# Kernel optimization log

Hardware: AMD Instinct MI355X
Metric: run time of the kernel (lower is better)

The kernel has to match this reference:

```python
import jax, jax.numpy as jnp
import numpy as np

DIM = 1024
HEADS = 16
DIM_HEAD = 64
INNER = HEADS * DIM_HEAD
THETA = 10000.0
EPS = 1e-5


def setup_inputs() -> dict:
    key = jax.random.key(0)
    k1, k2, k3, k4 = jax.random.split(key, 4)
    b, n = 4, 2048
    x = jax.random.normal(k1, (b, n, DIM), dtype=jnp.float32)
    gamma = jnp.ones((DIM,), jnp.float32)
    beta = jnp.zeros((DIM,), jnp.float32)
    w_qkv = jax.random.normal(k2, (DIM, 3 * INNER), dtype=jnp.float32) * (DIM ** -0.5)
    w_out = jax.random.normal(k3, (INNER, DIM), dtype=jnp.float32) * (INNER ** -0.5)
    b_out = jax.random.normal(k4, (DIM,), dtype=jnp.float32) * 0.01
    return {"x": x, "gamma": gamma, "beta": beta, "w_qkv": w_qkv, "w_out": w_out, "b_out": b_out}


def _rope_cos_sin(n, d, dtype):
    # freqs_cis = exp(i * t * theta^{-2j/d}) for j in [0, d/2)
    inv = 1.0 / (THETA ** (jnp.arange(0, d, 2, dtype=jnp.float32) / d))  # (d/2,)
    ang = jnp.arange(n, dtype=jnp.float32)[:, None] * inv[None, :]       # (n, d/2)
    return jnp.cos(ang).astype(dtype), jnp.sin(ang).astype(dtype)


def _apply_rope(t, cos, sin):
    # t: (b, n, h, d); rotate adjacent pairs along d
    b, n, h, d = t.shape
    tr = t.reshape(b, n, h, d // 2, 2)
    e, o = tr[..., 0], tr[..., 1]
    c = cos[None, :, None, :]
    s = sin[None, :, None, :]
    out = jnp.stack([e * c - o * s, e * s + o * c], axis=-1)
    return out.reshape(b, n, h, d)


def reference(x, gamma, beta, w_qkv, w_out, b_out):
    b, n, _ = x.shape
    # LayerNorm
    mu = jnp.mean(x, axis=-1, keepdims=True)
    var = jnp.mean(jnp.square(x - mu), axis=-1, keepdims=True)
    xn = (x - mu) * jax.lax.rsqrt(var + EPS) * gamma + beta
    # QKV projection (no bias)
    qkv = xn @ w_qkv  # (b, n, 3*INNER)
    q, k, v = jnp.split(qkv, 3, axis=-1)
    q = q.reshape(b, n, HEADS, DIM_HEAD)
    k = k.reshape(b, n, HEADS, DIM_HEAD)
    v = v.reshape(b, n, HEADS, DIM_HEAD)
    # RoPE on q, k (per head, global_start_pos = 0)
    cos, sin = _rope_cos_sin(n, DIM_HEAD, x.dtype)
    q = _apply_rope(q, cos, sin)
    k = _apply_rope(k, cos, sin)
    # attention
    scale = DIM_HEAD ** -0.5
    dots = jnp.einsum('bnhd,bmhd->bhnm', q, k) * scale
    attn = jax.nn.softmax(dots, axis=-1)
    out = jnp.einsum('bhnm,bmhd->bnhd', attn, v).reshape(b, n, INNER)
    return out @ w_out + b_out
```

## Files before the change

kernel.cpp:

```cpp
#include <hip/hip_runtime.h>
#include <hip/hip_fp16.h>

typedef __attribute__((ext_vector_type(8))) short short8;
typedef __attribute__((ext_vector_type(4))) short short4v;
typedef __attribute__((ext_vector_type(4))) float floatx4;
typedef _Float16 half8 __attribute__((ext_vector_type(8)));
typedef __fp16 fp16x2 __attribute__((ext_vector_type(2)));
typedef __attribute__((ext_vector_type(4))) unsigned uintx4;

extern "C" __device__ float __ocml_native_exp2_f32(float);

static __device__ __forceinline__ short f2h(float f) {
    _Float16 h = (_Float16)f;
    return __builtin_bit_cast(short, h);
}

static __device__ __forceinline__ unsigned pkrtz(float a, float b) {
    fp16x2 h = __builtin_amdgcn_cvt_pkrtz(a, b);
    return __builtin_bit_cast(unsigned, h);
}

static __device__ __forceinline__ void drain_all() { __builtin_amdgcn_s_waitcnt(0); }

static __device__ __forceinline__ floatx4 mfma16(short8 a, short8 b, floatx4 c) {
    return __builtin_amdgcn_mfma_f32_16x16x32_f16(__builtin_bit_cast(half8, a),
                                                  __builtin_bit_cast(half8, b), c, 0, 0, 0);
}

static __device__ __forceinline__ void async16(const void* g, void* l) {
    __builtin_amdgcn_global_load_lds((const __attribute__((address_space(1))) void*)g,
                                     (__attribute__((address_space(3))) void*)l, 16, 0, 0);
}

__global__ __launch_bounds__(256) void ln_kernel(const float* __restrict__ x,
                                                 const float* __restrict__ gamma,
                                                 const float* __restrict__ beta,
                                                 short* __restrict__ xh) {
    __shared__ float red[8];
    const int row = blockIdx.x, tid = threadIdx.x;
    const int w = tid >> 6, lane = tid & 63;
    const float4 v = ((const float4*)(x + (size_t)row * 1024))[tid];
    float s = v.x + v.y + v.z + v.w;
    float ss = v.x * v.x + v.y * v.y + v.z * v.z + v.w * v.w;
#pragma unroll
    for (int off = 32; off; off >>= 1) {
        s += __shfl_xor(s, off);
        ss += __shfl_xor(ss, off);
    }
    if (lane == 0) { red[w] = s; red[4 + w] = ss; }
    __syncthreads();
    s = red[0] + red[1] + red[2] + red[3];
    ss = red[4] + red[5] + red[6] + red[7];
    const float mu = s * (1.f / 1024.f);
    const float rs = rsqrtf(ss * (1.f / 1024.f) - mu * mu + 1e-5f);
    const float4 g = ((const float4*)gamma)[tid];
    const float4 bt = ((const float4*)beta)[tid];
    short4v ph;
    ph[0] = f2h((v.x - mu) * rs * g.x + bt.x);
    ph[1] = f2h((v.y - mu) * rs * g.y + bt.y);
    ph[2] = f2h((v.z - mu) * rs * g.z + bt.z);
    ph[3] = f2h((v.w - mu) * rs * g.w + bt.w);
    *(short4v*)(xh + (size_t)row * 1024 + tid * 4) = ph;
}

__global__ void tcast_h(const float* __restrict__ in, short* __restrict__ out, int R, int C) {
    __shared__ float t[32][33];
    const int bx = blockIdx.x * 32, by = blockIdx.y * 32;
    const int tx = threadIdx.x, ty = threadIdx.y;
#pragma unroll
    for (int i = 0; i < 32; i += 8) t[ty + i][tx] = in[(size_t)(by + ty + i) * C + bx + tx];
    __syncthreads();
#pragma unroll
    for (int i = 0; i < 32; i += 8) out[(size_t)(bx + ty + i) * R + by + tx] = f2h(t[tx][ty + i]);
}

__global__ __launch_bounds__(256, 4) void gemm_qkv(const short* __restrict__ A,
                                                   const short* __restrict__ BT,
                                                   short* __restrict__ Qd, short* __restrict__ Kd,
                                                   short* __restrict__ VTb) {
    extern __shared__ __align__(16) short pool[];
    short* sOut = pool;

    const int tid = threadIdx.x;
    const int w = tid >> 6, lane = tid & 63, quad = lane >> 4, l15 = lane & 15;
    const int wm = w >> 1, wn = w & 1;
    const int m0 = blockIdx.y * 128, n0 = blockIdx.x * 128;
    const int qsw = (quad ^ ((l15 >> 1) & 3)) * 8;

    int sr[2], skc[2];
#pragma unroll
    for (int i = 0; i < 2; ++i) {
        int c = i * 256 + tid;
        sr[i] = c >> 2;
        skc[i] = ((c & 3) ^ ((sr[i] >> 1) & 3)) << 3;
    }

    floatx4 acc[4][4];
#pragma unroll
    for (int i = 0; i < 4; i++)
#pragma unroll
        for (int j = 0; j < 4; j++) acc[i][j] = (floatx4){0.f, 0.f, 0.f, 0.f};

#pragma unroll
    for (int i = 0; i < 2; ++i) {
        int c = i * 256 + tid;
        async16(A + (size_t)(m0 + sr[i]) * 1024 + skc[i], (char*)pool + c * 16);
        async16(BT + (size_t)(n0 + sr[i]) * 1024 + skc[i], (char*)(pool + 4096) + c * 16);
    }
    drain_all();
    __syncthreads();

    for (int kt = 0; kt < 32; ++kt) {
        const short* cA = pool + (kt & 1) * 8192;
        const short* cB = cA + 4096;
        if (kt + 1 < 32) {
            short* nA = pool + ((kt + 1) & 1) * 8192;
            const int k0 = (kt + 1) * 32;
#pragma unroll
            for (int i = 0; i < 2; ++i) {
                int c = i * 256 + tid;
                async16(A + (size_t)(m0 + sr[i]) * 1024 + k0 + skc[i], (char*)nA + c * 16);
                async16(BT + (size_t)(n0 + sr[i]) * 1024 + k0 + skc[i], (char*)(nA + 4096) + c * 16);
            }
        }
        short8 af[4], bf[4];
#pragma unroll
        for (int t = 0; t < 4; t++) {
            af[t] = *(const short8*)(cA + (wm * 64 + t * 16 + l15) * 32 + qsw);
            bf[t] = *(const short8*)(cB + (wn * 64 + t * 16 + l15) * 32 + qsw);
        }
#pragma unroll
        for (int tm = 0; tm < 4; tm++)
#pragma unroll
            for (int tn = 0; tn < 4; tn++) acc[tm][tn] = mfma16(af[tm], bf[tn], acc[tm][tn]);
        drain_all();
        __syncthreads();
    }

    const int b = m0 >> 11, nnb = m0 & 2047;
    const bool isV = (n0 >= 2048);
    if (!isV) {
        const float qs = (n0 < 1024) ? 0.18033688011112042f : 1.0f;
#pragma unroll
        for (int tn = 0; tn < 4; tn++) {
            const int d = tn * 16 + l15;
            const int colL = wn * 64 + tn * 16 + l15;
            const float inv = exp2f((float)(d >> 1) * -0.4152410118609203f);
#pragma unroll
            for (int tm = 0; tm < 4; tm++) {
                const int rowL = wm * 64 + tm * 16 + quad * 4;
#pragma unroll
                for (int i = 0; i < 4; i++) {
                    float v = acc[tm][tn][i];
                    float pv = __shfl_xor(v, 1);
                    float ang = (float)(nnb + rowL + i) * inv;
                    float sn = __sinf(ang), cs = __cosf(ang);
                    float r = (d & 1) ? (pv * sn + v * cs) : (v * cs - pv * sn);
                    sOut[(rowL + i) * 136 + colL] = f2h(r * qs);
                }
            }
        }
        __syncthreads();
        short* dst0 = (n0 < 1024) ? Qd : Kd;
        const int hbase = (n0 & 1023) >> 6;
#pragma unroll
        for (int it = 0; it < 8; ++it) {
            int c = it * 256 + tid;
            int r = c >> 4, cg = (c & 15) * 8;
            int h = hbase + (cg >> 6), d = cg & 63;
            *(short8*)(dst0 + ((size_t)((b * 16 + h) * 2048 + nnb + r)) * 64 + d) =
                *(const short8*)(sOut + r * 136 + cg);
        }
    } else {
#pragma unroll
        for (int tn = 0; tn < 4; tn++) {
            const int colL = wn * 64 + tn * 16 + l15;
#pragma unroll
            for (int tm = 0; tm < 4; tm++) {
                const int rowL = wm * 64 + tm * 16 + quad * 4;
#pragma unroll
                for (int i = 0; i < 4; i++)
                    sOut[colL * 136 + rowL + i] = f2h(acc[tm][tn][i]);
            }
        }
        __syncthreads();
        const int hbase = (n0 & 1023) >> 6;
#pragma unroll
        for (int it = 0; it < 8; ++it) {
            int c = it * 256 + tid;
            int ci = c >> 4, rg = (c & 15) * 8;
            int h = hbase + (ci >> 6), d = ci & 63;
            short8 v = *(const short8*)(sOut + ci * 136 + rg);
            if (d & 8) v = __builtin_shufflevector(v, v, 4, 5, 6, 7, 0, 1, 2, 3);
            *(short8*)(VTb + ((size_t)((b * 16 + h) * 64 + d)) * 2048 + nnb + rg) = v;
        }
    }
}

__global__ __launch_bounds__(256, 4) void gemm_out(const short* __restrict__ A,
                                                   const short* __restrict__ BT,
                                                   float* __restrict__ Fout,
                                                   const float* __restrict__ bias) {
    __shared__ __align__(16) short pool2[16384];
    const int tid = threadIdx.x;
    const int w = tid >> 6, lane = tid & 63, quad = lane >> 4, l15 = lane & 15;
    const int wm = w >> 1, wn = w & 1;
    const int m0 = blockIdx.y * 128, n0 = blockIdx.x * 128;
    const int qsw = (quad ^ ((l15 >> 1) & 3)) * 8;

    int sr[2], skc[2];
#pragma unroll
    for (int i = 0; i < 2; ++i) {
        int c = i * 256 + tid;
        sr[i] = c >> 2;
        skc[i] = ((c & 3) ^ ((sr[i] >> 1) & 3)) << 3;
    }

    floatx4 acc[4][4];
#pragma unroll
    for (int i = 0; i < 4; i++)
#pragma unroll
        for (int j = 0; j < 4; j++) acc[i][j] = (floatx4){0.f, 0.f, 0.f, 0.f};

#pragma unroll
    for (int i = 0; i < 2; ++i) {
        int c = i * 256 + tid;
        async16(A + (size_t)(m0 + sr[i]) * 1024 + skc[i], (char*)pool2 + c * 16);
        async16(BT + (size_t)(n0 + sr[i]) * 1024 + skc[i], (char*)(pool2 + 4096) + c * 16);
    }
    drain_all();
    __syncthreads();

    for (int kt = 0; kt < 32; ++kt) {
        const short* cA = pool2 + (kt & 1) * 8192;
        const short* cB = cA + 4096;
        if (kt + 1 < 32) {
            short* nA = pool2 + ((kt + 1) & 1) * 8192;
            const int k0 = (kt + 1) * 32;
#pragma unroll
            for (int i = 0; i < 2; ++i) {
                int c = i * 256 + tid;
                async16(A + (size_t)(m0 + sr[i]) * 1024 + k0 + skc[i], (char*)nA + c * 16);
                async16(BT + (size_t)(n0 + sr[i]) * 1024 + k0 + skc[i], (char*)(nA + 4096) + c * 16);
            }
        }
        short8 af[4], bf[4];
#pragma unroll
        for (int t = 0; t < 4; t++) af[t] = *(const short8*)(cA + (wm * 64 + t * 16 + l15) * 32 + qsw);
#pragma unroll
        for (int t = 0; t < 4; t++) bf[t] = *(const short8*)(cB + (wn * 64 + t * 16 + l15) * 32 + qsw);
#pragma unroll
        for (int tm = 0; tm < 4; tm++)
#pragma unroll
            for (int tn = 0; tn < 4; tn++) acc[tm][tn] = mfma16(af[tm], bf[tn], acc[tm][tn]);
        drain_all();
        __syncthreads();
    }

#pragma unroll
    for (int tn = 0; tn < 4; tn++) {
        const int col = n0 + wn * 64 + tn * 16 + l15;
        const float bb = bias[col];
#pragma unroll
        for (int tm = 0; tm < 4; tm++) {
            const int row0 = m0 + wm * 64 + tm * 16 + quad * 4;
#pragma unroll
            for (int i = 0; i < 4; i++) Fout[(size_t)(row0 + i) * 1024 + col] = acc[tm][tn][i] + bb;
        }
    }
}

__global__ __launch_bounds__(512, 4) void attn_kernel(const short* __restrict__ Qg,
                                                      const short* __restrict__ Kg,
                                                      const short* __restrict__ VTg,
                                                      short* __restrict__ Og) {
    extern __shared__ __align__(16) short apool[];
    short* sKV0 = apool;
    short* sKV1 = apool + 8192;

    const int tid = threadIdx.x;
    const int w = tid >> 6, lane = tid & 63, quad = lane >> 4, l15 = lane & 15;
    const int qt = blockIdx.x, bh = blockIdx.y;

    const short* Qp = Qg + (size_t)(bh * 2048 + qt * 256) * 64;
    const short* Kp = Kg + (size_t)bh * 2048 * 64;
    const short* Vp = VTg + (size_t)bh * 64 * 2048;

    const int str = tid >> 3, stc = tid & 7;
    const int scl = stc ^ (str & 7);
    const int kSrcOff = str * 64 + scl * 8;
    const int vSrcOff = str * 2048 + scl * 8;
    const int dstOff = tid * 16;

    short8 aq[2][2];
#pragma unroll
    for (int rb = 0; rb < 2; rb++)
#pragma unroll
        for (int kh = 0; kh < 2; kh++)
            aq[rb][kh] = *(const short8*)(Qp + (w * 32 + rb * 16 + l15) * 64 + kh * 32 + quad * 8);

    short8 ones;
#pragma unroll
    for (int j = 0; j < 8; j++) ones[j] = 0x3C00;

    floatx4 o4[2][4], ol[2];
#pragma unroll
    for (int rb = 0; rb < 2; rb++) {
#pragma unroll
        for (int dt = 0; dt < 4; dt++) o4[rb][dt] = (floatx4){0.f, 0.f, 0.f, 0.f};
        ol[rb] = (floatx4){0.f, 0.f, 0.f, 0.f};
    }

    async16(Kp + kSrcOff, (char*)sKV0 + dstOff);
    async16(Vp + vSrcOff, (char*)(sKV0 + 4096) + dstOff);

    const int swz0 = (quad ^ (l15 & 7)) << 3;
    const int swz1 = ((4 | quad) ^ (l15 & 7)) << 3;

    for (int kt = 0; kt < 32; ++kt) {
        const short* sK = (kt & 1) ? sKV1 : sKV0;
        const short* sVT = sK + 4096;
        drain_all();
        __syncthreads();
        if (kt + 1 < 32) {
            short* nK = (kt & 1) ? sKV0 : sKV1;
            const int n0 = (kt + 1) * 64;
            async16(Kp + (size_t)n0 * 64 + kSrcOff, (char*)nK + dstOff);
            async16(Vp + n0 + vSrcOff, (char*)(nK + 4096) + dstOff);
        }

#pragma unroll
        for (int nc = 0; nc < 2; nc++) {
            floatx4 zA[2], zB[2];
            {
                const int rbase = ((2 * nc) * 16 + l15) * 64;
                short8 k0 = *(const short8*)(sK + rbase + swz0);
                short8 k1 = *(const short8*)(sK + rbase + swz1);
                __builtin_amdgcn_s_setprio(1);
#pragma unroll
                for (int rb = 0; rb < 2; rb++) {
                    floatx4 z = (floatx4){0.f, 0.f, 0.f, 0.f};
                    z = mfma16(k0, aq[rb][0], z);
                    z = mfma16(k1, aq[rb][1], z);
                    zA[rb] = z;
                }
                __builtin_amdgcn_s_setprio(0);
            }
            {
                const int rbase = ((2 * nc + 1) * 16 + l15) * 64;
                short8 k0 = *(const short8*)(sK + rbase + swz0);
                short8 k1 = *(const short8*)(sK + rbase + swz1);
                __builtin_amdgcn_s_setprio(1);
#pragma unroll
                for (int rb = 0; rb < 2; rb++) {
                    floatx4 z = (floatx4){0.f, 0.f, 0.f, 0.f};
                    z = mfma16(k0, aq[rb][0], z);
                    z = mfma16(k1, aq[rb][1], z);
                    zB[rb] = z;
                }
                __builtin_amdgcn_s_setprio(0);
            }

            short8 pa[4];
            const int r7 = l15 & 7;
            const int h4 = ((quad ^ (l15 >> 3)) & 1) << 2;
            const int cLo = (((nc << 2) | (quad >> 1)) ^ r7) << 3;
            const int cHi = ((((nc << 2) + 2) | (quad >> 1)) ^ r7) << 3;
#pragma unroll
            for (int dt = 0; dt < 4; dt++) {
                const short* rowp = sVT + (dt * 16 + l15) * 64;
                short4v lo = *(const short4v*)(rowp + cLo + h4);
                short4v hi = *(const short4v*)(rowp + cHi + h4);
                pa[dt] = __builtin_shufflevector(lo, hi, 0, 1, 2, 3, 4, 5, 6, 7);
            }

#pragma unroll
            for (int rb = 0; rb < 2; rb++) {
                uintx4 pbw;
                pbw.x = pkrtz(__ocml_native_exp2_f32(zA[rb][0]),
                              __ocml_native_exp2_f32(zA[rb][1]));
                pbw.y = pkrtz(__ocml_native_exp2_f32(zA[rb][2]),
                              __ocml_native_exp2_f32(zA[rb][3]));
                pbw.z = pkrtz(__ocml_native_exp2_f32(zB[rb][0]),
                              __ocml_native_exp2_f32(zB[rb][1]));
                pbw.w = pkrtz(__ocml_native_exp2_f32(zB[rb][2]),
                              __ocml_native_exp2_f32(zB[rb][3]));
                short8 pb = __builtin_bit_cast(short8, pbw);
                __builtin_amdgcn_s_setprio(1);
#pragma unroll
                for (int dt = 0; dt < 4; dt++) o4[rb][dt] = mfma16(pa[dt], pb, o4[rb][dt]);
                ol[rb] = mfma16(ones, pb, ol[rb]);
                __builtin_amdgcn_s_setprio(0);
            }
        }
    }

    float linv[2];
    linv[0] = 1.0f / ol[0][0];
    linv[1] = 1.0f / ol[1][0];

    drain_all();
    __syncthreads();
    short* sO = apool;
#pragma unroll
    for (int rb = 0; rb < 2; rb++) {
        const int q = w * 32 + rb * 16 + l15;
#pragma unroll
        for (int dt = 0; dt < 4; dt++) {
            short4v pk;
#pragma unroll
            for (int i = 0; i < 4; i++) pk[i] = f2h(o4[rb][dt][i] * linv[rb]);
            const int d0 = dt * 16 + quad * 4;
            *(short4v*)(sO + q * 64 + (((d0 >> 3) ^ (q & 7)) << 3) + (d0 & 7)) = pk;
        }
    }
    drain_all();
    __syncthreads();
    const int b = bh >> 4, h = bh & 15;
#pragma unroll
    for (int it = 0; it < 4; ++it) {
        int g = it * 512 + tid;
        int r = g >> 3, c = g & 7;
        *(short8*)(Og + (size_t)(b * 2048 + qt * 256 + r) * 1024 + h * 64 + c * 8) =
            *(const short8*)(sO + r * 64 + ((c ^ (r & 7)) << 3));
    }
}

extern "C" void kernel_launch(void* const* d_in, const int* in_sizes, int n_in, void* d_out,
                              int out_size, void* d_ws, size_t ws_size, hipStream_t stream) {
    const float* x = (const float*)d_in[0];
    const float* gamma = (const float*)d_in[1];
    const float* beta = (const float*)d_in[2];
    const float* w_qkv = (const float*)d_in[3];
    const float* w_out = (const float*)d_in[4];
    const float* b_out = (const float*)d_in[5];
    float* out = (float*)d_out;

    char* ws = (char*)d_ws;
    short* xh = (short*)ws;
    short* wqkvT = (short*)(ws + 16777216);
    short* woT = (short*)(ws + 23068672);
    short* VTb = (short*)(ws + 25165824);
    short* Qd = (short*)d_out;
    short* Kd = (short*)d_out + 8388608;

    ln_kernel<<<8192, 256, 0, stream>>>(x, gamma, beta, xh);
    tcast_h<<<dim3(96, 32), dim3(32, 8), 0, stream>>>(w_qkv, wqkvT, 1024, 3072);
    tcast_h<<<dim3(32, 32), dim3(32, 8), 0, stream>>>(w_out, woT, 1024, 1024);
    gemm_qkv<<<dim3(24, 64), 256, 34816, stream>>>(xh, wqkvT, Qd, Kd, VTb);
    attn_kernel<<<dim3(8, 64), 512, 32768, stream>>>(Qd, Kd, VTb, xh);
    gemm_out<<<dim3(8, 64), 256, 0, stream>>>(xh, woT, out, b_out);
}
```

Before: 266.3 us.

## Triple-buffer GEMM K-tiles with partial vmcnt waits and one barrier per step

Both projection GEMMs move from double-buffered LDS tiles with a full drain and two barriers per K-step to a three-stage ring. Loads are issued two tiles ahead, and each step waits only until the oldest tile has landed (vmcnt(4)) before a single barrier. This is meant to hide global-load latency behind MFMA work. In exchange, LDS use grows to 48KB per block and the occupancy hint drops from 4 to 3 blocks.

```diff
diff --git a/kernel.cpp b/kernel.cpp
--- a/kernel.cpp
+++ b/kernel.cpp
@@ -74,7 +74,7 @@
     for (int i = 0; i < 32; i += 8) out[(size_t)(bx + ty + i) * R + by + tx] = f2h(t[tx][ty + i]);
 }
 
-__global__ __launch_bounds__(256, 4) void gemm_qkv(const short* __restrict__ A,
+__global__ __launch_bounds__(256, 3) void gemm_qkv(const short* __restrict__ A,
                                                    const short* __restrict__ BT,
                                                    short* __restrict__ Qd, short* __restrict__ Kd,
                                                    short* __restrict__ VTb) {
@@ -107,22 +107,33 @@
         async16(A + (size_t)(m0 + sr[i]) * 1024 + skc[i], (char*)pool + c * 16);
         async16(BT + (size_t)(n0 + sr[i]) * 1024 + skc[i], (char*)(pool + 4096) + c * 16);
     }
-    drain_all();
-    __syncthreads();
+#pragma unroll
+    for (int i = 0; i < 2; ++i) {
+        int c = i * 256 + tid;
+        async16(A + (size_t)(m0 + sr[i]) * 1024 + 32 + skc[i], (char*)(pool + 8192) + c * 16);
+        async16(BT + (size_t)(n0 + sr[i]) * 1024 + 32 + skc[i], (char*)(pool + 12288) + c * 16);
+    }
 
     for (int kt = 0; kt < 32; ++kt) {
-        const short* cA = pool + (kt & 1) * 8192;
-        const short* cB = cA + 4096;
-        if (kt + 1 < 32) {
-            short* nA = pool + ((kt + 1) & 1) * 8192;
-            const int k0 = (kt + 1) * 32;
+        if (kt < 31) {
+            asm volatile("s_waitcnt vmcnt(4)" ::: "memory");
+        } else {
+            asm volatile("s_waitcnt vmcnt(0)" ::: "memory");
+        }
+        __builtin_amdgcn_sched_barrier(0);
+        __builtin_amdgcn_s_barrier();
+        if (kt + 2 < 32) {
+            short* nb = pool + ((kt + 2) % 3) * 8192;
+            const int k0 = (kt + 2) * 32;
 #pragma unroll
             for (int i = 0; i < 2; ++i) {
                 int c = i * 256 + tid;
-                async16(A + (size_t)(m0 + sr[i]) * 1024 + k0 + skc[i], (char*)nA + c * 16);
-                async16(BT + (size_t)(n0 + sr[i]) * 1024 + k0 + skc[i], (char*)(nA + 4096) + c * 16);
-            }
-        }
+                async16(A + (size_t)(m0 + sr[i]) * 1024 + k0 + skc[i], (char*)nb + c * 16);
+                async16(BT + (size_t)(n0 + sr[i]) * 1024 + k0 + skc[i], (char*)(nb + 4096) + c * 16);
+            }
+        }
+        const short* cA = pool + (kt % 3) * 8192;
+        const short* cB = cA + 4096;
         short8 af[4], bf[4];
 #pragma unroll
         for (int t = 0; t < 4; t++) {
@@ -133,9 +144,9 @@
         for (int tm = 0; tm < 4; tm++)
 #pragma unroll
             for (int tn = 0; tn < 4; tn++) acc[tm][tn] = mfma16(af[tm], bf[tn], acc[tm][tn]);
-        drain_all();
-        __syncthreads();
-    }
+    }
+
+    __syncthreads();
 
     const int b = m0 >> 11, nnb = m0 & 2047;
     const bool isV = (n0 >= 2048);
@@ -197,11 +208,11 @@
     }
 }
 
-__global__ __launch_bounds__(256, 4) void gemm_out(const short* __restrict__ A,
+__global__ __launch_bounds__(256, 3) void gemm_out(const short* __restrict__ A,
                                                    const short* __restrict__ BT,
                                                    float* __restrict__ Fout,
                                                    const float* __restrict__ bias) {
-    __shared__ __align__(16) short pool2[16384];
+    __shared__ __align__(16) short pool2[24576];
     const int tid = threadIdx.x;
     const int w = tid >> 6, lane = tid & 63, quad = lane >> 4, l15 = lane & 15;
     const int wm = w >> 1, wn = w & 1;
@@ -228,22 +239,33 @@
         async16(A + (size_t)(m0 + sr[i]) * 1024 + skc[i], (char*)pool2 + c * 16);
         async16(BT + (size_t)(n0 + sr[i]) * 1024 + skc[i], (char*)(pool2 + 4096) + c * 16);
     }
-    drain_all();
-    __syncthreads();
+#pragma unroll
+    for (int i = 0; i < 2; ++i) {
+        int c = i * 256 + tid;
+        async16(A + (size_t)(m0 + sr[i]) * 1024 + 32 + skc[i], (char*)(pool2 + 8192) + c * 16);
+        async16(BT + (size_t)(n0 + sr[i]) * 1024 + 32 + skc[i], (char*)(pool2 + 12288) + c * 16);
+    }
 
     for (int kt = 0; kt < 32; ++kt) {
-        const short* cA = pool2 + (kt & 1) * 8192;
-        const short* cB = cA + 4096;
-        if (kt + 1 < 32) {
-            short* nA = pool2 + ((kt + 1) & 1) * 8192;
-            const int k0 = (kt + 1) * 32;
+        if (kt < 31) {
+            asm volatile("s_waitcnt vmcnt(4)" ::: "memory");
+        } else {
+            asm volatile("s_waitcnt vmcnt(0)" ::: "memory");
+        }
+        __builtin_amdgcn_sched_barrier(0);
+        __builtin_amdgcn_s_barrier();
+        if (kt + 2 < 32) {
+            short* nb = pool2 + ((kt + 2) % 3) * 8192;
+            const int k0 = (kt + 2) * 32;
 #pragma unroll
             for (int i = 0; i < 2; ++i) {
                 int c = i * 256 + tid;
-                async16(A + (size_t)(m0 + sr[i]) * 1024 + k0 + skc[i], (char*)nA + c * 16);
-                async16(BT + (size_t)(n0 + sr[i]) * 1024 + k0 + skc[i], (char*)(nA + 4096) + c * 16);
-            }
-        }
+                async16(A + (size_t)(m0 + sr[i]) * 1024 + k0 + skc[i], (char*)nb + c * 16);
+                async16(BT + (size_t)(n0 + sr[i]) * 1024 + k0 + skc[i], (char*)(nb + 4096) + c * 16);
+            }
+        }
+        const short* cA = pool2 + (kt % 3) * 8192;
+        const short* cB = cA + 4096;
         short8 af[4], bf[4];
 #pragma unroll
         for (int t = 0; t < 4; t++) af[t] = *(const short8*)(cA + (wm * 64 + t * 16 + l15) * 32 + qsw);
@@ -253,8 +275,6 @@
         for (int tm = 0; tm < 4; tm++)
 #pragma unroll
             for (int tn = 0; tn < 4; tn++) acc[tm][tn] = mfma16(af[tm], bf[tn], acc[tm][tn]);
-        drain_all();
-        __syncthreads();
     }
 
 #pragma unroll
@@ -447,7 +467,7 @@
     ln_kernel<<<8192, 256, 0, stream>>>(x, gamma, beta, xh);
     tcast_h<<<dim3(96, 32), dim3(32, 8), 0, stream>>>(w_qkv, wqkvT, 1024, 3072);
     tcast_h<<<dim3(32, 32), dim3(32, 8), 0, stream>>>(w_out, woT, 1024, 1024);
-    gemm_qkv<<<dim3(24, 64), 256, 34816, stream>>>(xh, wqkvT, Qd, Kd, VTb);
+    gemm_qkv<<<dim3(24, 64), 256, 49152, stream>>>(xh, wqkvT, Qd, Kd, VTb);
     attn_kernel<<<dim3(8, 64), 512, 32768, stream>>>(Qd, Kd, VTb, xh);
     gemm_out<<<dim3(8, 64), 256, 0, stream>>>(xh, woT, out, b_out);
 }
```

New measurement: 269.1 us. No clear change (+1.1%).
